# Kernel tuning notes

Hardware: AMD Instinct MI355X
Metric: run time of the kernel (lower is better)

The kernel has to match this reference:

```python
import jax, jax.numpy as jnp
import numpy as np

N_ENT = 100000
N_USR = 30000
N_TOT = N_ENT + N_USR
N_REL = 32
D = 64
E = 500000
INTER = 500000
N_LAYERS = 2
SLOPE = 0.01  # torch nn.LeakyReLU default negative slope


def _seg_softmax(logits, seg, n):
    # sparse softmax over rows (segments)
    m = jax.ops.segment_max(logits, seg, num_segments=n)
    ex = jnp.exp(logits - m[seg])
    den = jax.ops.segment_sum(ex, seg, num_segments=n)
    return ex / den[seg]


def setup_inputs() -> dict:
    key = jax.random.key(0)
    k = jax.random.split(key, 14)
    all_embed = jax.random.normal(k[0], (N_TOT, D), jnp.float32) * 0.1
    rel_embed = jax.random.normal(k[1], (N_REL, D), jnp.float32) * 0.1
    Wk_w = jax.random.normal(k[2], (D, 2 * D), jnp.float32) / np.sqrt(2 * D)
    Wk_b = jnp.zeros((D,), jnp.float32)
    Wa_w = jax.random.normal(k[3], (D, D), jnp.float32) / np.sqrt(D)
    Wb_w = jax.random.normal(k[4], (D, D), jnp.float32) / np.sqrt(D)
    # KG edge lists (head entity, tail entity, relation)
    h_list = jnp.sort(jax.random.randint(k[5], (E,), 0, N_ENT))
    t_list = jax.random.randint(k[6], (E,), 0, N_ENT)
    r_list = jax.random.randint(k[7], (E,), 0, N_REL)
    # bipartite interaction matrix A_in (symmetric, items rows first then users)
    u = jax.random.randint(k[8], (INTER,), 0, N_USR)
    it = jax.random.randint(k[9], (INTER,), 0, N_ENT)
    a_row = jnp.concatenate([it, N_ENT + u])
    a_col = jnp.concatenate([N_ENT + u, it])
    a_vals = jax.random.uniform(k[10], (2 * INTER,), jnp.float32) * 0.01
    # calc_score ids: user ids are offset by n_entities in the concatenated table
    user_ids = N_ENT + jax.random.randint(k[11], (1024,), 0, N_USR)
    item_ids = jax.random.randint(k[12], (2048,), 0, N_ENT)
    return dict(all_embed=all_embed, rel_embed=rel_embed, Wk_w=Wk_w, Wk_b=Wk_b,
                Wa_w=Wa_w, Wb_w=Wb_w, a_vals=a_vals, user_ids=user_ids,
                item_ids=item_ids, h_list=h_list, t_list=t_list, r_list=r_list,
                a_row=a_row, a_col=a_col)


def _get_embeddings(all_embed, rel_embed, Wk_w, Wk_b, Wa_w, Wb_w, a_vals,
                    h_list, t_list, r_list, a_row, a_col):
    e_ent = all_embed[:N_ENT]
    e_usr = all_embed[N_ENT:]
    user_list = [e_usr]
    item_list = [e_ent]
    e_items_dual = e_ent
    e_users_curr = e_usr
    e_ent_curr = e_ent
    r_e = rel_embed[r_list]  # (E, D) -- constant across layers
    for _ in range(N_LAYERS):
        # --- KG attention (Eq. 2): gather + concat + linear + dot + leakyrelu ---
        h_e = e_ent_curr[h_list]            # (E, D)
        t_e = e_ent_curr[t_list]            # (E, D)
        cat = jnp.concatenate([t_e, h_e], axis=1)   # (E, 2D)
        trans = cat @ Wk_w.T + Wk_b                 # (E, D)
        logits = jnp.sum(trans * r_e, axis=1)       # (E,)
        vals = jnp.where(logits >= 0, logits, SLOPE * logits)
        alpha = _seg_softmax(vals, h_list, N_ENT)   # row-wise sparse softmax
        # --- KG aggregation (Eq. 1): spmm ---
        e_items_kg = jax.ops.segment_sum(alpha[:, None] * t_e, h_list,
                                         num_segments=N_ENT)
        # --- IG aggregation (Eq. 3 & 6): spmm with A_in ---
        ig_in = jnp.concatenate([e_items_dual, e_users_curr], axis=0)  # (N_TOT, D)
        ig_out = jax.ops.segment_sum(a_vals[:, None] * ig_in[a_col], a_row,
                                     num_segments=N_TOT)
        e_items_collab = ig_out[:N_ENT]
        e_users_new = ig_out[N_ENT:]
        # --- fusion gate (Eq. 4, 5) ---
        g = jax.nn.sigmoid(e_items_kg @ Wa_w.T + e_items_collab @ Wb_w.T)
        e_items_dual = g * e_items_kg + (1.0 - g) * e_items_collab
        item_list.append(e_items_collab)
        user_list.append(e_users_new)
        e_users_curr = e_users_new
        e_ent_curr = e_items_kg
    item_final = sum(item_list)
    user_final = sum(user_list)
    return jnp.concatenate([item_final, user_final], axis=0)


def reference(all_embed, rel_embed, Wk_w, Wk_b, Wa_w, Wb_w, a_vals,
              user_ids, item_ids, h_list, t_list, r_list, a_row, a_col):
    all_final = _get_embeddings(all_embed, rel_embed, Wk_w, Wk_b, Wa_w, Wb_w,
                                a_vals, h_list, t_list, r_list, a_row, a_col)
    user_e = all_final[user_ids]   # (Bu, D)
    item_e = all_final[item_ids]   # (Bi, D)
    return user_e @ item_e.T       # (Bu, Bi)
```

## Files before the change

kernel.cpp:

```cpp
#include <hip/hip_runtime.h>
#include <hip/hip_bf16.h>

#define N_ENT 100000
#define N_USR 30000
#define N_TOTN 130000
#define N_RELC 32
#define DIM 64
#define NEDGE 500000
#define INTER 500000
#define SLOPE 0.01f
#define CPT_NB 127
#define FILL_NB 489
#define MARK_NB 489
#define ATT_NB 1024
#define RSTR 64
#define KGOFF_NB 1954

typedef unsigned char u8;
typedef unsigned long long u64;

__device__ __forceinline__ float grp_sum16(float v){
  v += __shfl_xor(v, 8, 64);
  v += __shfl_xor(v, 4, 64);
  v += __shfl_xor(v, 2, 64);
  v += __shfl_xor(v, 1, 64);
  return v;
}

__global__ void __launch_bounds__(256) k_prep(
    const float* __restrict__ rel, const float* __restrict__ Wk,
    const float* __restrict__ Wkb, float* __restrict__ m, float* __restrict__ b,
    const int* __restrict__ user_ids, const int* __restrict__ item_ids,
    u8* __restrict__ r2_item, u8* __restrict__ r2_user,
    const int* __restrict__ h_list, int* __restrict__ off){
  int bid = blockIdx.x;
  if (bid < 17){
    int idx = bid*256 + threadIdx.x;
    if (idx < N_RELC*128){
      int r = idx >> 7, j = idx & 127;
      float s = 0.f;
      for (int d = 0; d < DIM; ++d) s += rel[r*DIM+d] * Wk[d*128+j];
      m[idx] = s;
    } else if (idx < N_RELC*128 + N_RELC){
      int r = idx - N_RELC*128;
      float s = 0.f;
      for (int d = 0; d < DIM; ++d) s += Wkb[d] * rel[r*DIM+d];
      b[r] = s;
    }
  } else if (bid < 29){
    int i = (bid - 17)*256 + threadIdx.x;
    if (i < 1024) r2_user[user_ids[i] - N_ENT] = 1;
    else if (i < 3072) r2_item[item_ids[i - 1024]] = 1;
  } else {
    int e = (bid - 29)*256 + threadIdx.x;
    if (e <= NEDGE){
      int hc = (e < NEDGE) ? h_list[e] : N_ENT;
      int hp = (e == 0) ? -1 : h_list[e-1];
      for (int s = hp+1; s <= hc; ++s) off[s] = e;
    }
  }
}

__global__ void k_mark(const int4* __restrict__ a_row4, const int4* __restrict__ a_col4,
                       const u8* __restrict__ r2_item, const u8* __restrict__ r2_user,
                       u8* __restrict__ need_d, u8* __restrict__ need_u){
  int i = blockIdx.x*256 + threadIdx.x;
  if (i >= INTER/4) return;
  int4 ar = a_row4[i];
  int4 ac = a_col4[i];
  #pragma unroll
  for (int k = 0; k < 4; ++k){
    int it = (&ar.x)[k];
    int uu = (&ac.x)[k] - N_ENT;
    if (r2_item[it]) need_u[uu] = 1;
    if (r2_user[uu]) need_d[it] = 1;
  }
}

__global__ void __launch_bounds__(256) k_buildfill(
    const int* __restrict__ a_row, const int* __restrict__ a_col,
    const float* __restrict__ a_vals,
    const u8* __restrict__ need_d, const u8* __restrict__ need_u,
    const u8* __restrict__ r2_item, const u8* __restrict__ r2_user,
    int* __restrict__ list_gate, int* __restrict__ list_s1,
    int* __restrict__ counters, int* __restrict__ cnt, int2* __restrict__ csr){
  if (blockIdx.x < CPT_NB){
    __shared__ u64 mg_sh[16], ms_sh[16];
    __shared__ int pre_g[16], pre_s[16];
    __shared__ int base_sh[2];
    int t = threadIdx.x;
    int wave = t >> 6, lane = t & 63;
    bool pg[4], ps[4];
    int ibase = blockIdx.x*1024;
    #pragma unroll
    for (int k = 0; k < 4; ++k){
      int i = ibase + k*256 + t;
      bool g = false, s = false;
      if (i < N_TOTN){
        if (i < N_ENT){ g = need_d[i] != 0; s = g || (r2_item[i] != 0); }
        else { int u = i - N_ENT; s = (need_u[u] != 0) || (r2_user[u] != 0); }
      }
      pg[k] = g; ps[k] = s;
      u64 mg = __ballot(g), ms = __ballot(s);
      if (lane == 0){ mg_sh[k*4 + wave] = mg; ms_sh[k*4 + wave] = ms; }
    }
    __syncthreads();
    if (t == 0){
      int sg = 0, ss = 0;
      for (int j = 0; j < 16; ++j){
        pre_g[j] = sg; sg += __popcll(mg_sh[j]);
        pre_s[j] = ss; ss += __popcll(ms_sh[j]);
      }
      base_sh[0] = sg ? atomicAdd(&counters[0], sg) : 0;
      base_sh[1] = ss ? atomicAdd(&counters[1], ss) : 0;
    }
    __syncthreads();
    int bg = base_sh[0], bs = base_sh[1];
    u64 lmask = (1ull << lane) - 1;
    #pragma unroll
    for (int k = 0; k < 4; ++k){
      int i = ibase + k*256 + t;
      if (pg[k]) list_gate[bg + pre_g[k*4+wave] + __popcll(mg_sh[k*4+wave] & lmask)] = i;
      if (ps[k]) list_s1 [bs + pre_s[k*4+wave] + __popcll(ms_sh[k*4+wave] & lmask)] = i;
    }
  } else {
    int i = (blockIdx.x - CPT_NB)*256 + threadIdx.x;
    if (i >= INTER/4) return;
    int4 ar = ((const int4*)a_row)[i];
    int4 ac = ((const int4*)a_col)[i];
    float4 av0 = ((const float4*)a_vals)[i];
    float4 av1 = ((const float4*)(a_vals + INTER))[i];
    #pragma unroll
    for (int k = 0; k < 4; ++k){
      int it = (&ar.x)[k];
      int uc = (&ac.x)[k];
      int uu = uc - N_ENT;
      if (need_d[it] | r2_item[it]){
        int p = atomicAdd(&cnt[it], 1);
        if (p < RSTR) csr[((size_t)it << 6) + p] = make_int2(uc, __float_as_int((&av0.x)[k]));
      }
      if (need_u[uu] | r2_user[uu]){
        int p = atomicAdd(&cnt[uc], 1);
        if (p < RSTR) csr[((size_t)uc << 6) + p] = make_int2(it, __float_as_int((&av1.x)[k]));
      }
    }
  }
}

__global__ void __launch_bounds__(256) k_l1(const float4* __restrict__ ent4,
    const float4* __restrict__ m4, const float* __restrict__ bvec,
    const int* __restrict__ off, const int* __restrict__ t_list,
    const int* __restrict__ r_list, const int* __restrict__ list_gate,
    const int* __restrict__ list_s1, const int* __restrict__ counters,
    float4* __restrict__ kg4, const int* __restrict__ cnt,
    const int2* __restrict__ csr,
    float4* __restrict__ collab4, float4* __restrict__ x2_4){
  if (blockIdx.x < ATT_NB){
    __shared__ float4 msh[N_RELC*32];
    __shared__ float bsh[N_RELC];
    for (int i = threadIdx.x; i < N_RELC*32; i += 256) msh[i] = m4[i];
    if (threadIdx.x < N_RELC) bsh[threadIdx.x] = bvec[threadIdx.x];
    __syncthreads();
    int n = counters[0];
    int sub = threadIdx.x & 15;
    int grp = (blockIdx.x*256 + threadIdx.x) >> 4;
    int ng = (ATT_NB*256) >> 4;
    for (int idx = grp; idx < n; idx += ng){
      int s = list_gate[idx];
      int beg = off[s], end = off[s+1];
      float4 h4 = ent4[(size_t)s*16 + sub];
      float l = 0.f;
      float4 acc = {0.f,0.f,0.f,0.f};
      for (int base = beg; base < end; base += 16){
        int mch = end - base; if (mch > 16) mch = 16;
        int tj = 0, rj = 0;
        if (sub < mch){ tj = t_list[base + sub]; rj = r_list[base + sub]; }
        #pragma unroll 4
        for (int j = 0; j < mch; ++j){
          int ti = __shfl(tj, j, 16);
          int r  = __shfl(rj, j, 16);
          float4 t4 = ent4[(size_t)ti*16 + sub];
          float4 mt = msh[r*32 + sub];
          float4 mh = msh[r*32 + 16 + sub];
          float v = t4.x*mt.x + t4.y*mt.y + t4.z*mt.z + t4.w*mt.w
                  + h4.x*mh.x + h4.y*mh.y + h4.z*mh.z + h4.w*mh.w;
          v = grp_sum16(v) + bsh[r];
          v = (v >= 0.f) ? v : SLOPE * v;
          float w = __expf(v);
          l += w;
          acc.x += w*t4.x; acc.y += w*t4.y; acc.z += w*t4.z; acc.w += w*t4.w;
        }
      }
      float inv = (end > beg) ? 1.f / l : 0.f;
      float4 o = {acc.x*inv, acc.y*inv, acc.z*inv, acc.w*inv};
      kg4[(size_t)s*16 + sub] = o;
    }
  } else {
    int n = counters[1];
    int sub = threadIdx.x & 15;
    int bid = blockIdx.x - ATT_NB;
    int nb = gridDim.x - ATT_NB;
    int grp = (bid*256 + threadIdx.x) >> 4;
    int ng = (nb*256) >> 4;
    for (int idx = grp; idx < n; idx += ng){
      int i = list_s1[idx];
      int deg = cnt[i]; if (deg > RSTR) deg = RSTR;
      size_t base0 = (size_t)i << 6;
      float4 acc = {0.f,0.f,0.f,0.f};
      for (int b = 0; b < deg; b += 16){
        int mch = deg - b; if (mch > 16) mch = 16;
        int2 e = make_int2(0, 0);
        if (sub < mch) e = csr[base0 + b + sub];
        #pragma unroll 4
        for (int j = 0; j < mch; ++j){
          int cj = __shfl(e.x, j, 16);
          float vj = __int_as_float(__shfl(e.y, j, 16));
          float4 sv = ent4[(size_t)cj*16 + sub];
          acc.x += vj*sv.x; acc.y += vj*sv.y; acc.z += vj*sv.z; acc.w += vj*sv.w;
        }
      }
      if (i < N_ENT) collab4[(size_t)i*16 + sub] = acc;
      else x2_4[(size_t)i*16 + sub] = acc;
    }
  }
}

__global__ void __launch_bounds__(256) k_gate(const float* __restrict__ kg,
    const float* __restrict__ collab, const float* __restrict__ Wa,
    const float* __restrict__ Wb, float* __restrict__ x2dual,
    const int* __restrict__ list, const int* __restrict__ counters){
  int n = counters[0];
  __shared__ float Xsh[64][129];
  __shared__ float Wsh[128][65];
  for (int i = threadIdx.x; i < 64*64; i += 256){
    int a = i >> 6, j = i & 63;
    Wsh[j][a] = Wa[i];
    Wsh[64 + j][a] = Wb[i];
  }
  int ct = threadIdx.x & 15, rt = threadIdx.x >> 4;
  int r0 = rt * 4, c0 = ct * 4;
  for (int row0 = blockIdx.x*64; row0 < n; row0 += gridDim.x*64){
    __syncthreads();
    for (int i = threadIdx.x; i < 64*128; i += 256){
      int r = i >> 7, c = i & 127;
      int idx = row0 + r;
      float v = 0.f;
      if (idx < n){
        int row = list[idx];
        v = (c < 64) ? kg[(size_t)row*64 + c] : collab[(size_t)row*64 + (c - 64)];
      }
      Xsh[r][c] = v;
    }
    __syncthreads();
    float acc[4][4] = {};
    for (int k = 0; k < 128; ++k){
      float w0 = Wsh[k][c0], w1 = Wsh[k][c0+1], w2 = Wsh[k][c0+2], w3 = Wsh[k][c0+3];
      #pragma unroll
      for (int i = 0; i < 4; ++i){
        float x = Xsh[r0+i][k];
        acc[i][0] += x*w0; acc[i][1] += x*w1; acc[i][2] += x*w2; acc[i][3] += x*w3;
      }
    }
    #pragma unroll
    for (int i = 0; i < 4; ++i){
      int idx = row0 + r0 + i;
      if (idx < n){
        int row = list[idx];
        float4 o;
        #pragma unroll
        for (int j = 0; j < 4; ++j){
          int c = c0 + j;
          float g = 1.f / (1.f + __expf(-acc[i][j]));
          float kv = Xsh[r0+i][c];
          float cv = Xsh[r0+i][64 + c];
          (&o.x)[j] = g*kv + (1.f - g)*cv;
        }
        *(float4*)&x2dual[(size_t)row*64 + c0] = o;
      }
    }
  }
}

__global__ void __launch_bounds__(256) k_spmm2g(const int* __restrict__ cnt,
    const int2* __restrict__ csr, const float* __restrict__ x2,
    const float* __restrict__ all_embed, const float* __restrict__ collab1,
    const int* __restrict__ user_ids, const int* __restrict__ item_ids,
    float* __restrict__ user_e, float* __restrict__ item_e){
  int lane = threadIdx.x & 63;
  int g = (blockIdx.x*256 + threadIdx.x) >> 6;
  if (g >= 3072) return;
  int id;
  float b1;
  if (g < 1024){
    id = user_ids[g];
    b1 = x2[(size_t)id*64 + lane];
  } else {
    id = item_ids[g - 1024];
    b1 = collab1[(size_t)id*64 + lane];
  }
  float acc = all_embed[(size_t)id*64 + lane] + b1;
  int deg = cnt[id]; if (deg > RSTR) deg = RSTR;
  size_t base0 = (size_t)id << 6;
  int2 e = make_int2(0, 0);
  if (lane < deg) e = csr[base0 + lane];
  #pragma unroll 4
  for (int j = 0; j < deg; ++j){
    int cj = __shfl(e.x, j, 64);
    float vj = __int_as_float(__shfl(e.y, j, 64));
    acc += vj * x2[(size_t)cj*64 + lane];
  }
  if (g < 1024) user_e[(size_t)g*64 + lane] = acc;
  else item_e[(size_t)(g - 1024)*64 + lane] = acc;
}

__global__ void __launch_bounds__(256) k_out(const float* __restrict__ ue,
    const float* __restrict__ ie, float* __restrict__ out){
  __shared__ float ash[64][65];
  __shared__ float bsh[64][65];
  int row0 = blockIdx.y * 64, col0 = blockIdx.x * 64;
  for (int i = threadIdx.x; i < 64*64; i += 256){
    int r = i >> 6, c = i & 63;
    ash[r][c] = ue[(size_t)(row0 + r)*DIM + c];
    bsh[r][c] = ie[(size_t)(col0 + r)*DIM + c];
  }
  __syncthreads();
  int tx = threadIdx.x & 15, ty = threadIdx.x >> 4;
  int r0 = ty*4, c0 = tx*4;
  float acc[4][4] = {};
  #pragma unroll
  for (int k = 0; k < 64; ++k){
    float a0 = ash[r0][k], a1 = ash[r0+1][k], a2 = ash[r0+2][k], a3 = ash[r0+3][k];
    float b0 = bsh[c0][k], b1 = bsh[c0+1][k], b2 = bsh[c0+2][k], b3 = bsh[c0+3][k];
    acc[0][0] += a0*b0; acc[0][1] += a0*b1; acc[0][2] += a0*b2; acc[0][3] += a0*b3;
    acc[1][0] += a1*b0; acc[1][1] += a1*b1; acc[1][2] += a1*b2; acc[1][3] += a1*b3;
    acc[2][0] += a2*b0; acc[2][1] += a2*b1; acc[2][2] += a2*b2; acc[2][3] += a2*b3;
    acc[3][0] += a3*b0; acc[3][1] += a3*b1; acc[3][2] += a3*b2; acc[3][3] += a3*b3;
  }
  #pragma unroll
  for (int i = 0; i < 4; ++i){
    float4 o = {acc[i][0], acc[i][1], acc[i][2], acc[i][3]};
    *(float4*)&out[(size_t)(row0 + r0 + i)*2048 + col0 + c0] = o;
  }
}

extern "C" void kernel_launch(void* const* d_in, const int* in_sizes, int n_in,
                              void* d_out, int out_size, void* d_ws, size_t ws_size,
                              hipStream_t stream){
  const float* all_embed = (const float*)d_in[0];
  const float* rel_embed = (const float*)d_in[1];
  const float* Wk_w      = (const float*)d_in[2];
  const float* Wk_b      = (const float*)d_in[3];
  const float* Wa_w      = (const float*)d_in[4];
  const float* Wb_w      = (const float*)d_in[5];
  const float* a_vals    = (const float*)d_in[6];
  const int* user_ids   = (const int*)d_in[7];
  const int* item_ids   = (const int*)d_in[8];
  const int* h_list     = (const int*)d_in[9];
  const int* t_list     = (const int*)d_in[10];
  const int* r_list     = (const int*)d_in[11];
  const int* a_row      = (const int*)d_in[12];
  const int* a_col      = (const int*)d_in[13];
  float* out = (float*)d_out;

  char* p = (char*)d_ws;
  auto alloc = [&](size_t bytes)->void*{
    void* r = (void*)p;
    p += (bytes + 255) & ~(size_t)255;
    return r;
  };
  float* m_rel   = (float*)alloc((size_t)N_RELC*128*4);
  float* b_rel   = (float*)alloc((size_t)N_RELC*4);
  int*   kg_off  = (int*)  alloc((size_t)(N_ENT+1)*4);
  size_t zbytes = (size_t)N_TOTN*4 + 256 + (2*(size_t)N_ENT + 2*(size_t)N_USR);
  char*  zbase  = (char*)alloc(zbytes);
  int*   cnt      = (int*)zbase;
  int*   counters = (int*)(zbase + (size_t)N_TOTN*4);
  u8*    r2_item  = (u8*)(zbase + (size_t)N_TOTN*4 + 256);
  u8*    r2_user  = r2_item + N_ENT;
  u8*    need_d   = r2_user + N_USR;
  u8*    need_u   = need_d + N_ENT;
  int2*  csr     = (int2*) alloc((size_t)N_TOTN*RSTR*8);
  int*   list_gate = (int*)alloc((size_t)N_ENT*4);
  int*   list_s1   = (int*)alloc((size_t)N_TOTN*4);
  float* kg1     = (float*)alloc((size_t)N_ENT*DIM*4);
  float* collab1 = (float*)alloc((size_t)N_ENT*DIM*4);
  float* x2      = (float*)alloc((size_t)N_TOTN*DIM*4);
  float* user_e  = (float*)alloc((size_t)1024*DIM*4);
  float* item_e  = (float*)alloc((size_t)2048*DIM*4);

  hipMemsetAsync(zbase, 0, zbytes, stream);
  k_prep<<<29 + KGOFF_NB, 256, 0, stream>>>(rel_embed, Wk_w, Wk_b,
      m_rel, b_rel, user_ids, item_ids, r2_item, r2_user, h_list, kg_off);
  k_mark<<<MARK_NB, 256, 0, stream>>>((const int4*)a_row, (const int4*)a_col,
      r2_item, r2_user, need_d, need_u);
  k_buildfill<<<CPT_NB + FILL_NB, 256, 0, stream>>>(a_row, a_col, a_vals,
      need_d, need_u, r2_item, r2_user, list_gate, list_s1, counters, cnt, csr);

  k_l1<<<ATT_NB + 2048, 256, 0, stream>>>((const float4*)all_embed,
      (const float4*)m_rel, b_rel, kg_off, t_list, r_list, list_gate, list_s1,
      counters, (float4*)kg1, cnt, csr, (float4*)collab1, (float4*)x2);
  k_gate<<<256, 256, 0, stream>>>(kg1, collab1, Wa_w, Wb_w, x2,
      list_gate, counters);
  k_spmm2g<<<768, 256, 0, stream>>>(cnt, csr, x2, all_embed, collab1,
      user_ids, item_ids, user_e, item_e);
  dim3 grid_out(2048/64, 1024/64);
  k_out<<<grid_out, 256, 0, stream>>>(user_e, item_e, out);
}
```

Baseline: 198.7 us.

## Fuse fusion gate and item collab SpMM into KG attention kernel

The separate gate kernel is folded into the KG attention path. Each 16-lane group now computes the KG aggregate, the collaborative SpMM row and the sigmoid gate for its entity, then writes collab and the gated dual embedding directly. This drops the kg1 intermediate buffer and one kernel launch. Gate entities are excluded from the generic SpMM list, and that branch's grid is halved. The trade-off is extra shared memory for transposed Wa/Wb in every block, plus more serial work per attention group, which could lower occupancy.

After: 200.0 us. Within noise of the previous version (+0.6%).

```diff
diff --git a/kernel.cpp b/kernel.cpp
--- a/kernel.cpp
+++ b/kernel.cpp
@@ -1,5 +1,4 @@
 #include <hip/hip_runtime.h>
-#include <hip/hip_bf16.h>
 
 #define N_ENT 100000
 #define N_USR 30000
@@ -13,6 +12,7 @@
 #define FILL_NB 489
 #define MARK_NB 489
 #define ATT_NB 1024
+#define SP_NB 1024
 #define RSTR 64
 #define KGOFF_NB 1954
 
@@ -97,7 +97,7 @@
       int i = ibase + k*256 + t;
       bool g = false, s = false;
       if (i < N_TOTN){
-        if (i < N_ENT){ g = need_d[i] != 0; s = g || (r2_item[i] != 0); }
+        if (i < N_ENT){ g = need_d[i] != 0; s = (!g) && (r2_item[i] != 0); }
         else { int u = i - N_ENT; s = (need_u[u] != 0) || (r2_user[u] != 0); }
       }
       pg[k] = g; ps[k] = s;
@@ -147,19 +147,26 @@
   }
 }
 
-__global__ void __launch_bounds__(256) k_l1(const float4* __restrict__ ent4,
+__global__ void __launch_bounds__(256) k_l1g(const float4* __restrict__ ent4,
     const float4* __restrict__ m4, const float* __restrict__ bvec,
+    const float* __restrict__ Wa, const float* __restrict__ Wb,
     const int* __restrict__ off, const int* __restrict__ t_list,
     const int* __restrict__ r_list, const int* __restrict__ list_gate,
     const int* __restrict__ list_s1, const int* __restrict__ counters,
-    float4* __restrict__ kg4, const int* __restrict__ cnt,
-    const int2* __restrict__ csr,
+    const int* __restrict__ cnt, const int2* __restrict__ csr,
     float4* __restrict__ collab4, float4* __restrict__ x2_4){
+  __shared__ float4 msh[N_RELC*32];
+  __shared__ float bsh[N_RELC];
+  __shared__ float WaT[64][65];
+  __shared__ float WbT[64][65];
   if (blockIdx.x < ATT_NB){
-    __shared__ float4 msh[N_RELC*32];
-    __shared__ float bsh[N_RELC];
     for (int i = threadIdx.x; i < N_RELC*32; i += 256) msh[i] = m4[i];
     if (threadIdx.x < N_RELC) bsh[threadIdx.x] = bvec[threadIdx.x];
+    for (int i = threadIdx.x; i < 64*64; i += 256){
+      int d = i >> 6, k = i & 63;
+      WaT[k][d] = Wa[i];
+      WbT[k][d] = Wb[i];
+    }
     __syncthreads();
     int n = counters[0];
     int sub = threadIdx.x & 15;
@@ -192,8 +199,47 @@
         }
       }
       float inv = (end > beg) ? 1.f / l : 0.f;
-      float4 o = {acc.x*inv, acc.y*inv, acc.z*inv, acc.w*inv};
-      kg4[(size_t)s*16 + sub] = o;
+      float4 kg = {acc.x*inv, acc.y*inv, acc.z*inv, acc.w*inv};
+      int deg = cnt[s]; if (deg > RSTR) deg = RSTR;
+      size_t base0 = (size_t)s << 6;
+      float4 cb = {0.f,0.f,0.f,0.f};
+      for (int b = 0; b < deg; b += 16){
+        int mch = deg - b; if (mch > 16) mch = 16;
+        int2 e = make_int2(0, 0);
+        if (sub < mch) e = csr[base0 + b + sub];
+        #pragma unroll 4
+        for (int j = 0; j < mch; ++j){
+          int cj = __shfl(e.x, j, 16);
+          float vj = __int_as_float(__shfl(e.y, j, 16));
+          float4 sv = ent4[(size_t)cj*16 + sub];
+          cb.x += vj*sv.x; cb.y += vj*sv.y; cb.z += vj*sv.z; cb.w += vj*sv.w;
+        }
+      }
+      int d0 = sub*4;
+      float4 ga = {0.f,0.f,0.f,0.f};
+      for (int kk = 0; kk < 16; ++kk){
+        float kqx = __shfl(kg.x, kk, 16), kqy = __shfl(kg.y, kk, 16);
+        float kqz = __shfl(kg.z, kk, 16), kqw = __shfl(kg.w, kk, 16);
+        float cqx = __shfl(cb.x, kk, 16), cqy = __shfl(cb.y, kk, 16);
+        float cqz = __shfl(cb.z, kk, 16), cqw = __shfl(cb.w, kk, 16);
+        int k0 = kk*4;
+        #pragma unroll
+        for (int j = 0; j < 4; ++j){
+          float tsum = kqx*WaT[k0][d0+j] + kqy*WaT[k0+1][d0+j]
+                     + kqz*WaT[k0+2][d0+j] + kqw*WaT[k0+3][d0+j]
+                     + cqx*WbT[k0][d0+j] + cqy*WbT[k0+1][d0+j]
+                     + cqz*WbT[k0+2][d0+j] + cqw*WbT[k0+3][d0+j];
+          (&ga.x)[j] += tsum;
+        }
+      }
+      float4 o;
+      #pragma unroll
+      for (int j = 0; j < 4; ++j){
+        float g = 1.f / (1.f + __expf(-(&ga.x)[j]));
+        (&o.x)[j] = g*(&kg.x)[j] + (1.f - g)*(&cb.x)[j];
+      }
+      collab4[(size_t)s*16 + sub] = cb;
+      x2_4[(size_t)s*16 + sub] = o;
     }
   } else {
     int n = counters[1];
@@ -225,62 +271,6 @@
   }
 }
 
-__global__ void __launch_bounds__(256) k_gate(const float* __restrict__ kg,
-    const float* __restrict__ collab, const float* __restrict__ Wa,
-    const float* __restrict__ Wb, float* __restrict__ x2dual,
-    const int* __restrict__ list, const int* __restrict__ counters){
-  int n = counters[0];
-  __shared__ float Xsh[64][129];
-  __shared__ float Wsh[128][65];
-  for (int i = threadIdx.x; i < 64*64; i += 256){
-    int a = i >> 6, j = i & 63;
-    Wsh[j][a] = Wa[i];
-    Wsh[64 + j][a] = Wb[i];
-  }
-  int ct = threadIdx.x & 15, rt = threadIdx.x >> 4;
-  int r0 = rt * 4, c0 = ct * 4;
-  for (int row0 = blockIdx.x*64; row0 < n; row0 += gridDim.x*64){
-    __syncthreads();
-    for (int i = threadIdx.x; i < 64*128; i += 256){
-      int r = i >> 7, c = i & 127;
-      int idx = row0 + r;
-      float v = 0.f;
-      if (idx < n){
-        int row = list[idx];
-        v = (c < 64) ? kg[(size_t)row*64 + c] : collab[(size_t)row*64 + (c - 64)];
-      }
-      Xsh[r][c] = v;
-    }
-    __syncthreads();
-    float acc[4][4] = {};
-    for (int k = 0; k < 128; ++k){
-      float w0 = Wsh[k][c0], w1 = Wsh[k][c0+1], w2 = Wsh[k][c0+2], w3 = Wsh[k][c0+3];
-      #pragma unroll
-      for (int i = 0; i < 4; ++i){
-        float x = Xsh[r0+i][k];
-        acc[i][0] += x*w0; acc[i][1] += x*w1; acc[i][2] += x*w2; acc[i][3] += x*w3;
-      }
-    }
-    #pragma unroll
-    for (int i = 0; i < 4; ++i){
-      int idx = row0 + r0 + i;
-      if (idx < n){
-        int row = list[idx];
-        float4 o;
-        #pragma unroll
-        for (int j = 0; j < 4; ++j){
-          int c = c0 + j;
-          float g = 1.f / (1.f + __expf(-acc[i][j]));
-          float kv = Xsh[r0+i][c];
-          float cv = Xsh[r0+i][64 + c];
-          (&o.x)[j] = g*kv + (1.f - g)*cv;
-        }
-        *(float4*)&x2dual[(size_t)row*64 + c0] = o;
-      }
-    }
-  }
-}
-
 __global__ void __launch_bounds__(256) k_spmm2g(const int* __restrict__ cnt,
     const int2* __restrict__ csr, const float* __restrict__ x2,
     const float* __restrict__ all_embed, const float* __restrict__ collab1,
@@ -382,7 +372,6 @@
   int2*  csr     = (int2*) alloc((size_t)N_TOTN*RSTR*8);
   int*   list_gate = (int*)alloc((size_t)N_ENT*4);
   int*   list_s1   = (int*)alloc((size_t)N_TOTN*4);
-  float* kg1     = (float*)alloc((size_t)N_ENT*DIM*4);
   float* collab1 = (float*)alloc((size_t)N_ENT*DIM*4);
   float* x2      = (float*)alloc((size_t)N_TOTN*DIM*4);
   float* user_e  = (float*)alloc((size_t)1024*DIM*4);
@@ -396,11 +385,10 @@
   k_buildfill<<<CPT_NB + FILL_NB, 256, 0, stream>>>(a_row, a_col, a_vals,
       need_d, need_u, r2_item, r2_user, list_gate, list_s1, counters, cnt, csr);
 
-  k_l1<<<ATT_NB + 2048, 256, 0, stream>>>((const float4*)all_embed,
-      (const float4*)m_rel, b_rel, kg_off, t_list, r_list, list_gate, list_s1,
-      counters, (float4*)kg1, cnt, csr, (float4*)collab1, (float4*)x2);
-  k_gate<<<256, 256, 0, stream>>>(kg1, collab1, Wa_w, Wb_w, x2,
-      list_gate, counters);
+  k_l1g<<<ATT_NB + SP_NB, 256, 0, stream>>>((const float4*)all_embed,
+      (const float4*)m_rel, b_rel, Wa_w, Wb_w, kg_off, t_list, r_list,
+      list_gate, list_s1, counters, cnt, csr, (float4*)collab1, (float4*)x2);
+
   k_spmm2g<<<768, 256, 0, stream>>>(cnt, csr, x2, all_embed, collab1,
       user_ids, item_ids, user_e, item_e);
   dim3 grid_out(2048/64, 1024/64);
```
